# Kernel optimization log

Measured on AMD Instinct MI355X. Metric: run time of the kernel, lower is better.

The kernel has to match this reference:

```python
import jax, jax.numpy as jnp
import numpy as np

N = 50000      # nodes
E = 800000     # edges (before self loops)
D_IN = 128
D_H = 128
HEADS = 4
C = D_H // HEADS
D_OUT = 64
G = 50         # graphs in batch
EPS = 1e-5


def setup_inputs() -> dict:
    key = jax.random.key(0)
    ks = jax.random.split(key, 40)
    def rn(k, shape, scale=0.05):
        return jax.random.normal(k, shape, jnp.float32) * scale
    inp = {}
    inp['x'] = jax.random.normal(ks[0], (N, D_IN), jnp.float32)
    inp['edge_index'] = jax.random.randint(ks[1], (2, E), 0, N, dtype=jnp.int32)
    inp['batch'] = jnp.sort(jax.random.randint(ks[2], (N,), 0, G, dtype=jnp.int32))
    # GATConv 1 (in=D_IN, heads=4, out-per-head=C, concat)
    inp['gat1_W'] = rn(ks[3], (D_IN, D_H))
    inp['gat1_as'] = rn(ks[4], (HEADS, C))
    inp['gat1_ad'] = rn(ks[5], (HEADS, C))
    inp['gat1_b'] = rn(ks[6], (D_H,))
    # GATConv 2 (in=D_H)
    inp['gat2_W'] = rn(ks[7], (D_H, D_H))
    inp['gat2_as'] = rn(ks[8], (HEADS, C))
    inp['gat2_ad'] = rn(ks[9], (HEADS, C))
    inp['gat2_b'] = rn(ks[10], (D_H,))
    # SAGEConv 3/4/5: lin_l (aggregated neighbors, has bias), lin_r (root, no bias)
    for i, kk in zip((3, 4, 5), (11, 14, 17)):
        inp[f'sage{i}_Wl'] = rn(ks[kk], (D_H, D_H))
        inp[f'sage{i}_bl'] = rn(ks[kk + 1], (D_H,))
        inp[f'sage{i}_Wr'] = rn(ks[kk + 2], (D_H, D_H))
    # BatchNorms (training-mode batch statistics)
    for i in range(1, 6):
        inp[f'bn{i}_g'] = jnp.ones((D_H,), jnp.float32)
        inp[f'bn{i}_b'] = jnp.zeros((D_H,), jnp.float32)
    # residual projections + final fc
    inp['res1_W'] = rn(ks[20], (D_IN, D_H)); inp['res1_b'] = rn(ks[21], (D_H,))
    inp['res2_W'] = rn(ks[22], (D_H, D_H)); inp['res2_b'] = rn(ks[23], (D_H,))
    inp['fc_W'] = rn(ks[24], (D_H, D_OUT)); inp['fc_b'] = rn(ks[25], (D_OUT,))
    return inp


def _segsum(v, idx, n):
    return jax.ops.segment_sum(v, idx, num_segments=n)


def _gat(x, W, a_src, a_dst, b, src, dst):
    # PyG GATConv with self loops already appended to (src, dst).
    h = (x @ W).reshape(N, HEADS, C)
    es = jnp.einsum('nhc,hc->nh', h, a_src)           # [N,H]
    ed = jnp.einsum('nhc,hc->nh', h, a_dst)
    e = jax.nn.leaky_relu(es[src] + ed[dst], 0.2)     # [Etot,H]
    m = jax.ops.segment_max(e, dst, num_segments=N)
    m = jnp.where(jnp.isfinite(m), m, 0.0)
    w = jnp.exp(e - m[dst])
    z = _segsum(w, dst, N)
    alpha = w / jnp.maximum(z[dst], 1e-16)            # edge softmax over dst
    out = _segsum(h[src] * alpha[:, :, None], dst, N)  # [N,H,C]
    return out.reshape(N, D_H) + b


def _sage(x, Wl, bl, Wr, src, dst):
    # PyG SAGEConv(aggr='mean'): lin_l(mean_neighbors) + lin_r(x)
    deg = _segsum(jnp.ones((src.shape[0],), x.dtype), dst, N)
    mean = _segsum(x[src], dst, N) / jnp.maximum(deg, 1.0)[:, None]
    return mean @ Wl + bl + x @ Wr


def _bn(x, g, b):
    mu = x.mean(0)
    var = x.var(0)
    return g * (x - mu) * jax.lax.rsqrt(var + EPS) + b


def reference(x, edge_index, batch,
              gat1_W, gat1_as, gat1_ad, gat1_b,
              gat2_W, gat2_as, gat2_ad, gat2_b,
              sage3_Wl, sage3_bl, sage3_Wr,
              sage4_Wl, sage4_bl, sage4_Wr,
              sage5_Wl, sage5_bl, sage5_Wr,
              bn1_g, bn1_b, bn2_g, bn2_b, bn3_g, bn3_b, bn4_g, bn4_b, bn5_g, bn5_b,
              res1_W, res1_b, res2_W, res2_b, fc_W, fc_b):
    src, dst = edge_index[0], edge_index[1]
    loops = jnp.arange(N, dtype=edge_index.dtype)
    gsrc = jnp.concatenate([src, loops])   # GATConv adds self loops by default
    gdst = jnp.concatenate([dst, loops])
    lrelu = lambda v: jax.nn.leaky_relu(v, 0.2)

    res1 = x @ res1_W + res1_b
    h = _gat(x, gat1_W, gat1_as, gat1_ad, gat1_b, gsrc, gdst)
    h = lrelu(_bn(h, bn1_g, bn1_b) + res1)            # dropout = identity (eval)

    res2 = h @ res2_W + res2_b
    h = _gat(h, gat2_W, gat2_as, gat2_ad, gat2_b, gsrc, gdst)
    h = lrelu(_bn(h, bn2_g, bn2_b) + res2)

    h = lrelu(_bn(_sage(h, sage3_Wl, sage3_bl, sage3_Wr, src, dst), bn3_g, bn3_b))
    h = lrelu(_bn(_sage(h, sage4_Wl, sage4_bl, sage4_Wr, src, dst), bn4_g, bn4_b))
    h = lrelu(_bn(_sage(h, sage5_Wl, sage5_bl, sage5_Wr, src, dst), bn5_g, bn5_b))

    # global_mean_pool over graphs
    cnt = jax.ops.segment_sum(jnp.ones((N,), h.dtype), batch, num_segments=G)
    pooled = jax.ops.segment_sum(h, batch, num_segments=G) / jnp.maximum(cnt, 1.0)[:, None]
    return pooled @ fc_W + fc_b
```

## Files before the change

kernel.cpp:

```cpp
#include <hip/hip_runtime.h>
#include <math.h>
#include <stdint.h>

#define N_NODES 50000
#define N_EDGES 800000
#define D 128
#define GR 50
#define EPSV 1e-5f

typedef __attribute__((ext_vector_type(8))) short bf16x8;
typedef __attribute__((ext_vector_type(4))) float f32x4;

__device__ __forceinline__ float lrelu(float v){ return v > 0.f ? v : 0.2f*v; }

__device__ __forceinline__ unsigned int f2bf(float f){
  union { float f; uint32_t i; } v; v.f = f;
  uint32_t r = v.i + 0x7fffu + ((v.i >> 16) & 1u);
  return r >> 16;
}
__device__ __forceinline__ float2 bf2f2(uint32_t u){
  union { uint32_t i; float f; } a, b;
  a.i = u << 16;
  b.i = u & 0xffff0000u;
  return make_float2(a.f, b.f);
}

__global__ void k_countrank(const int* __restrict__ dst, int* __restrict__ deg,
                            int* __restrict__ rank){
  int e = blockIdx.x*256 + threadIdx.x;
  if (e < N_EDGES) rank[e] = atomicAdd(&deg[dst[e]], 1);
}
__global__ void k_scan1(const int* __restrict__ deg, int* __restrict__ bsum){
  __shared__ int s[256];
  int i = blockIdx.x*256 + threadIdx.x;
  int v = (i < N_NODES) ? deg[i] : 0;
  s[threadIdx.x] = v; __syncthreads();
  for (int off = 128; off > 0; off >>= 1){
    if (threadIdx.x < off) s[threadIdx.x] += s[threadIdx.x + off];
    __syncthreads();
  }
  if (threadIdx.x == 0) bsum[blockIdx.x] = s[0];
}
__global__ void k_scan2b(int* __restrict__ bsum, int nb, int* __restrict__ rowStart){
  __shared__ int s[256];
  int t = threadIdx.x;
  int v = (t < nb) ? bsum[t] : 0;
  s[t] = v; __syncthreads();
  for (int off = 1; off < 256; off <<= 1){
    int xv = (t >= off) ? s[t - off] : 0;
    __syncthreads();
    s[t] += xv;
    __syncthreads();
  }
  if (t < nb) bsum[t] = s[t] - v;
  if (t == 255) rowStart[N_NODES] = s[255];
}
__global__ void k_scan3(const int* __restrict__ deg, const int* __restrict__ bsum,
                        int* __restrict__ rowStart){
  __shared__ int s[256];
  int i = blockIdx.x*256 + threadIdx.x;
  int v = (i < N_NODES) ? deg[i] : 0;
  s[threadIdx.x] = v; __syncthreads();
  for (int off = 1; off < 256; off <<= 1){
    int xv = (threadIdx.x >= off) ? s[threadIdx.x - off] : 0;
    __syncthreads();
    s[threadIdx.x] += xv;
    __syncthreads();
  }
  if (i < N_NODES) rowStart[i] = bsum[blockIdx.x] + s[threadIdx.x] - v;
}
__global__ void k_scatter(const int* __restrict__ src, const int* __restrict__ dst,
                          const int* __restrict__ rank, const int* __restrict__ rowStart,
                          int* __restrict__ srcList){
  int e = blockIdx.x*256 + threadIdx.x;
  if (e < N_EDGES)
    srcList[rowStart[dst[e]] + rank[e]] = src[e];
}

__global__ void k_cast_x(const float* __restrict__ x, unsigned short* __restrict__ x16){
  int idx = blockIdx.x*256 + threadIdx.x;
  if (idx >= N_NODES*32) return;
  float4 v = *(const float4*)(x + (size_t)idx*4);
  uint2 pk;
  pk.x = f2bf(v.x) | (f2bf(v.y) << 16);
  pk.y = f2bf(v.z) | (f2bf(v.w) << 16);
  *(uint2*)(x16 + (size_t)idx*4) = pk;
}

struct WPack { const float* w[10]; };
__global__ void k_castw(WPack p, unsigned short* __restrict__ wt){
  int mat = blockIdx.x >> 6;
  int local = (blockIdx.x & 63)*256 + threadIdx.x;
  int c = local >> 7, k = local & 127;
  wt[(size_t)mat*16384 + c*128 + k] = (unsigned short)f2bf(p.w[mat][k*128 + c]);
}

__device__ __forceinline__ void stage_w(const unsigned short* __restrict__ wt,
                                        unsigned short* __restrict__ lds, int t){
  #pragma unroll
  for (int i = 0; i < 8; ++i){
    int ch = i*256 + t;
    int col = ch >> 4, kc = ch & 15;
    *(uint4*)(&lds[col*136 + kc*8]) = *(const uint4*)(wt + ((size_t)col << 7) + (kc << 3));
  }
}

__device__ __forceinline__ void load_a(const unsigned short* __restrict__ xrow,
                                       int quad, bf16x8 a[4]){
  #pragma unroll
  for (int ks = 0; ks < 4; ++ks)
    a[ks] = *(const bf16x8*)(xrow + ks*32 + quad*8);
}

__device__ __forceinline__ void mfma_regs(const bf16x8 a[4],
                                          const unsigned short* __restrict__ lds,
                                          int lane, f32x4 acc[8]){
  int quad = lane >> 4, m = lane & 15;
  #pragma unroll
  for (int ks = 0; ks < 4; ++ks){
    #pragma unroll
    for (int nt = 0; nt < 8; ++nt){
      bf16x8 b = *(const bf16x8*)(&lds[(nt*16 + m)*136 + ks*32 + quad*8]);
      acc[nt] = __builtin_amdgcn_mfma_f32_16x16x32_bf16(a[ks], b, acc[nt], 0, 0, 0);
    }
  }
}

__device__ __forceinline__ void epi_store16(f32x4 acc[8], const float* bias,
    unsigned short* __restrict__ ldsw, unsigned short* __restrict__ Y16,
    int rbase, int lane, int n){
  int quad = lane >> 4, m = lane & 15;
  #pragma unroll
  for (int nt = 0; nt < 8; ++nt){
    int col = nt*16 + m;
    float bv = bias ? bias[col] : 0.f;
    #pragma unroll
    for (int reg = 0; reg < 4; ++reg)
      ldsw[(quad*4 + reg)*132 + col] = (unsigned short)f2bf(acc[nt][reg] + bv);
  }
  int r = lane >> 2, seg = lane & 3;
  int grow = rbase + r;
  if (grow < n){
    unsigned short* gp = Y16 + (size_t)grow*128 + seg*32;
    #pragma unroll
    for (int j = 0; j < 4; ++j)
      *(uint4*)(gp + j*8) = *(const uint4*)(&ldsw[r*132 + seg*32 + j*8]);
  }
}

__global__ __launch_bounds__(256) void k_mgemm(const unsigned short* __restrict__ X16,
    const unsigned short* __restrict__ wt, const float* __restrict__ bias,
    unsigned short* __restrict__ Y16, int n){
  __shared__ __align__(16) unsigned short Wlds[128*136];
  int t = threadIdx.x, lane = t & 63, w = t >> 6;
  int quad = lane >> 4, m = lane & 15;
  int rbase = blockIdx.x*64 + w*16;
  int rowA = rbase + m; if (rowA >= n) rowA = n - 1;
  bf16x8 a[4];
  load_a(X16 + (size_t)rowA*128, quad, a);
  stage_w(wt, Wlds, t);
  f32x4 acc[8];
  #pragma unroll
  for (int nt = 0; nt < 8; ++nt){ acc[nt][0]=0.f; acc[nt][1]=0.f; acc[nt][2]=0.f; acc[nt][3]=0.f; }
  __syncthreads();
  mfma_regs(a, Wlds, lane, acc);
  __syncthreads();
  epi_store16(acc, bias, Wlds + w*2112, Y16, rbase, lane, n);
}

__global__ __launch_bounds__(256) void k_mgemm_gat(const unsigned short* __restrict__ X16,
    const unsigned short* __restrict__ wt, const float* __restrict__ as_,
    const float* __restrict__ ad_, unsigned short* __restrict__ H16,
    float* __restrict__ es, float* __restrict__ ed, int n){
  __shared__ __align__(16) unsigned short Wlds[128*136];
  int t = threadIdx.x, lane = t & 63, w = t >> 6;
  int quad = lane >> 4, m = lane & 15;
  int rbase = blockIdx.x*64 + w*16;
  int rowA = rbase + m; if (rowA >= n) rowA = n - 1;
  bf16x8 a[4];
  load_a(X16 + (size_t)rowA*128, quad, a);
  stage_w(wt, Wlds, t);
  f32x4 acc[8];
  #pragma unroll
  for (int nt = 0; nt < 8; ++nt){ acc[nt][0]=0.f; acc[nt][1]=0.f; acc[nt][2]=0.f; acc[nt][3]=0.f; }
  __syncthreads();
  mfma_regs(a, Wlds, lane, acc);

  float asv[8], adv[8];
  #pragma unroll
  for (int nt = 0; nt < 8; ++nt){ asv[nt] = as_[nt*16 + m]; adv[nt] = ad_[nt*16 + m]; }
  #pragma unroll
  for (int reg = 0; reg < 4; ++reg){
    int row = rbase + quad*4 + reg;
    float pe[4], pd[4];
    #pragma unroll
    for (int h = 0; h < 4; ++h){
      pe[h] = acc[2*h][reg]*asv[2*h] + acc[2*h+1][reg]*asv[2*h+1];
      pd[h] = acc[2*h][reg]*adv[2*h] + acc[2*h+1][reg]*adv[2*h+1];
    }
    #pragma unroll
    for (int h = 0; h < 4; ++h){
      pe[h] += __shfl_xor(pe[h], 1); pe[h] += __shfl_xor(pe[h], 2);
      pe[h] += __shfl_xor(pe[h], 4); pe[h] += __shfl_xor(pe[h], 8);
      pd[h] += __shfl_xor(pd[h], 1); pd[h] += __shfl_xor(pd[h], 2);
      pd[h] += __shfl_xor(pd[h], 4); pd[h] += __shfl_xor(pd[h], 8);
    }
    if (m == 0 && row < n){
      #pragma unroll
      for (int h = 0; h < 4; ++h){ es[row*4 + h] = pe[h]; ed[row*4 + h] = pd[h]; }
    }
  }
  __syncthreads();
  epi_store16(acc, nullptr, Wlds + w*2112, H16, rbase, lane, n);
}

__global__ __launch_bounds__(256) void k_mgemm2(const unsigned short* __restrict__ Xa,
    const unsigned short* __restrict__ wta, const unsigned short* __restrict__ Xb,
    const unsigned short* __restrict__ wtb, const float* __restrict__ bias,
    unsigned short* __restrict__ Y16, int n, float* __restrict__ bnpart){
  __shared__ __align__(16) unsigned short Wlds[128*136];
  __shared__ float wredS[4][128], wredQ[4][128];
  int t = threadIdx.x, lane = t & 63, w = t >> 6;
  int quad = lane >> 4, m = lane & 15;
  int rbase = blockIdx.x*64 + w*16;
  int rowA = rbase + m; if (rowA >= n) rowA = n - 1;
  bf16x8 aa[4], ab[4];
  load_a(Xa + (size_t)rowA*128, quad, aa);
  load_a(Xb + (size_t)rowA*128, quad, ab);
  stage_w(wta, Wlds, t);
  f32x4 acc[8];
  #pragma unroll
  for (int nt = 0; nt < 8; ++nt){ acc[nt][0]=0.f; acc[nt][1]=0.f; acc[nt][2]=0.f; acc[nt][3]=0.f; }
  __syncthreads();
  mfma_regs(aa, Wlds, lane, acc);
  __syncthreads();
  stage_w(wtb, Wlds, t);
  __syncthreads();
  mfma_regs(ab, Wlds, lane, acc);

  float colS[8], colQ[8];
  #pragma unroll
  for (int nt = 0; nt < 8; ++nt){
    float bv = bias[nt*16 + m];
    float s = 0.f, q = 0.f;
    #pragma unroll
    for (int reg = 0; reg < 4; ++reg){
      float o = acc[nt][reg] + bv;
      acc[nt][reg] = o;
      if (rbase + quad*4 + reg < n){ s += o; q += o*o; }
    }
    s += __shfl_xor(s, 16); s += __shfl_xor(s, 32);
    q += __shfl_xor(q, 16); q += __shfl_xor(q, 32);
    colS[nt] = s; colQ[nt] = q;
  }
  if (quad == 0){
    #pragma unroll
    for (int nt = 0; nt < 8; ++nt){
      wredS[w][nt*16 + m] = colS[nt];
      wredQ[w][nt*16 + m] = colQ[nt];
    }
  }
  __syncthreads();
  if (t < 128){
    float S = wredS[0][t] + wredS[1][t] + wredS[2][t] + wredS[3][t];
    float Q = wredQ[0][t] + wredQ[1][t] + wredQ[2][t] + wredQ[3][t];
    bnpart[(size_t)blockIdx.x*256 + t]       = S;
    bnpart[(size_t)blockIdx.x*256 + 128 + t] = Q;
  }
  epi_store16(acc, nullptr, Wlds + w*2112, Y16, rbase, lane, n);
}

__global__ void k_bnred(const float* __restrict__ part, int nblk,
                        float* __restrict__ sums){
  int g = blockIdx.x, t = threadIdx.x;
  int chunk = (nblk + 63) / 64;
  int b0 = g*chunk, b1 = min(nblk, b0 + chunk);
  float s = 0.f;
  for (int b = b0; b < b1; ++b) s += part[(size_t)b*256 + t];
  if (b0 < b1) atomicAdd(&sums[t], s);
}

__global__ __launch_bounds__(256) void k_gat(const uint4* __restrict__ h16,
    const float* __restrict__ es, const float* __restrict__ edv,
    const int* __restrict__ rowStart, const int* __restrict__ srcList,
    const float* __restrict__ bias, uint4* __restrict__ out16){
  int i = blockIdx.x*4 + (threadIdx.x >> 6);
  if (i >= N_NODES) return;
  int lane = threadIdx.x & 63;
  int sub = lane >> 4;
  int m   = lane & 15;
  int hd  = m >> 2;
  float edi = edv[i*4 + hd];
  float acc[8];
  #pragma unroll
  for (int j = 0; j < 8; ++j) acc[j] = 0.f;
  float z = 0.f;
  if (sub == 0){
    float ws = __expf(lrelu(es[i*4 + hd] + edi));
    uint4 u = h16[(size_t)i*16 + m];
    float2 v0=bf2f2(u.x), v1=bf2f2(u.y), v2=bf2f2(u.z), v3=bf2f2(u.w);
    acc[0]=v0.x*ws; acc[1]=v0.y*ws; acc[2]=v1.x*ws; acc[3]=v1.y*ws;
    acc[4]=v2.x*ws; acc[5]=v2.y*ws; acc[6]=v3.x*ws; acc[7]=v3.y*ws;
    z = ws;
  }
  int k0 = rowStart[i], ke = rowStart[i + 1];
  for (int k = k0; k < ke; k += 8){
    int e0 = k + sub, e1 = k + 4 + sub;
    int c0 = e0 < ke ? e0 : ke - 1;
    int c1 = e1 < ke ? e1 : ke - 1;
    int s0 = srcList[c0];
    int s1 = srcList[c1];
    uint4 u0 = h16[(size_t)s0*16 + m];
    uint4 u1 = h16[(size_t)s1*16 + m];
    float w0 = (e0 < ke) ? __expf(lrelu(es[s0*4 + hd] + edi)) : 0.f;
    float w1 = (e1 < ke) ? __expf(lrelu(es[s1*4 + hd] + edi)) : 0.f;
    z += w0 + w1;
    float2 a0=bf2f2(u0.x), a1=bf2f2(u0.y), a2=bf2f2(u0.z), a3=bf2f2(u0.w);
    float2 b0=bf2f2(u1.x), b1=bf2f2(u1.y), b2=bf2f2(u1.z), b3=bf2f2(u1.w);
    acc[0] += a0.x*w0 + b0.x*w1;  acc[1] += a0.y*w0 + b0.y*w1;
    acc[2] += a1.x*w0 + b1.x*w1;  acc[3] += a1.y*w0 + b1.y*w1;
    acc[4] += a2.x*w0 + b2.x*w1;  acc[5] += a2.y*w0 + b2.y*w1;
    acc[6] += a3.x*w0 + b3.x*w1;  acc[7] += a3.y*w0 + b3.y*w1;
  }
  #pragma unroll
  for (int j = 0; j < 8; ++j){
    acc[j] += __shfl_xor(acc[j], 16);
    acc[j] += __shfl_xor(acc[j], 32);
  }
  z += __shfl_xor(z, 16);
  z += __shfl_xor(z, 32);
  if (sub == 0){
    float inv = 1.f / z;
    float4 bv0 = *(const float4*)(bias + m*8);
    float4 bv1 = *(const float4*)(bias + m*8 + 4);
    uint4 pk;
    pk.x = f2bf(acc[0]*inv + bv0.x) | (f2bf(acc[1]*inv + bv0.y) << 16);
    pk.y = f2bf(acc[2]*inv + bv0.z) | (f2bf(acc[3]*inv + bv0.w) << 16);
    pk.z = f2bf(acc[4]*inv + bv1.x) | (f2bf(acc[5]*inv + bv1.y) << 16);
    pk.w = f2bf(acc[6]*inv + bv1.z) | (f2bf(acc[7]*inv + bv1.w) << 16);
    out16[(size_t)i*16 + m] = pk;
  }
}

__global__ __launch_bounds__(256) void k_sage_mean(const uint4* __restrict__ h16,
    const int* __restrict__ rowStart, const int* __restrict__ srcList,
    uint4* __restrict__ out16){
  int i = blockIdx.x*4 + (threadIdx.x >> 6);
  if (i >= N_NODES) return;
  int lane = threadIdx.x & 63;
  int sub = lane >> 4;
  int m   = lane & 15;
  float acc[8];
  #pragma unroll
  for (int j = 0; j < 8; ++j) acc[j] = 0.f;
  int k0 = rowStart[i], ke = rowStart[i + 1];
  for (int k = k0; k < ke; k += 8){
    int e0 = k + sub, e1 = k + 4 + sub;
    int c0 = e0 < ke ? e0 : ke - 1;
    int c1 = e1 < ke ? e1 : ke - 1;
    int s0 = srcList[c0];
    int s1 = srcList[c1];
    uint4 u0 = h16[(size_t)s0*16 + m];
    uint4 u1 = h16[(size_t)s1*16 + m];
    float w0 = (e0 < ke) ? 1.f : 0.f;
    float w1 = (e1 < ke) ? 1.f : 0.f;
    float2 a0=bf2f2(u0.x), a1=bf2f2(u0.y), a2=bf2f2(u0.z), a3=bf2f2(u0.w);
    float2 b0=bf2f2(u1.x), b1=bf2f2(u1.y), b2=bf2f2(u1.z), b3=bf2f2(u1.w);
    acc[0] += a0.x*w0 + b0.x*w1;  acc[1] += a0.y*w0 + b0.y*w1;
    acc[2] += a1.x*w0 + b1.x*w1;  acc[3] += a1.y*w0 + b1.y*w1;
    acc[4] += a2.x*w0 + b2.x*w1;  acc[5] += a2.y*w0 + b2.y*w1;
    acc[6] += a3.x*w0 + b3.x*w1;  acc[7] += a3.y*w0 + b3.y*w1;
  }
  #pragma unroll
  for (int j = 0; j < 8; ++j){
    acc[j] += __shfl_xor(acc[j], 16);
    acc[j] += __shfl_xor(acc[j], 32);
  }
  if (sub == 0){
    int dg = ke - k0;
    float inv = 1.f / (float)(dg > 0 ? dg : 1);
    uint4 pk;
    pk.x = f2bf(acc[0]*inv) | (f2bf(acc[1]*inv) << 16);
    pk.y = f2bf(acc[2]*inv) | (f2bf(acc[3]*inv) << 16);
    pk.z = f2bf(acc[4]*inv) | (f2bf(acc[5]*inv) << 16);
    pk.w = f2bf(acc[6]*inv) | (f2bf(acc[7]*inv) << 16);
    out16[(size_t)i*16 + m] = pk;
  }
}

__global__ __launch_bounds__(256) void k_bnstat(const unsigned int* __restrict__ x16,
                                                float* __restrict__ sums){
  int colu = threadIdx.x & 63;
  int ro   = threadIdx.x >> 6;
  float s0 = 0.f, s1 = 0.f, q0 = 0.f, q1 = 0.f;
  for (int r = blockIdx.x*4 + ro; r < N_NODES; r += gridDim.x*4){
    float2 v = bf2f2(x16[(size_t)r*64 + colu]);
    s0 += v.x; s1 += v.y; q0 += v.x*v.x; q1 += v.y*v.y;
  }
  __shared__ float rs0[256], rs1[256], rq0[256], rq1[256];
  int t = threadIdx.x;
  rs0[t] = s0; rs1[t] = s1; rq0[t] = q0; rq1[t] = q1;
  __syncthreads();
  if (t < 64){
    float S0 = rs0[t] + rs0[t+64] + rs0[t+128] + rs0[t+192];
    float S1 = rs1[t] + rs1[t+64] + rs1[t+128] + rs1[t+192];
    float Q0 = rq0[t] + rq0[t+64] + rq0[t+128] + rq0[t+192];
    float Q1 = rq1[t] + rq1[t+64] + rq1[t+128] + rq1[t+192];
    atomicAdd(&sums[2*t],       S0);
    atomicAdd(&sums[2*t + 1],   S1);
    atomicAdd(&sums[128 + 2*t],     Q0);
    atomicAdd(&sums[128 + 2*t + 1], Q1);
  }
}

__global__ void k_bnapply(const unsigned int* __restrict__ x16,
    const float* __restrict__ sums, const float* __restrict__ g,
    const float* __restrict__ b, const unsigned int* __restrict__ res16,
    unsigned int* __restrict__ y16){
  int f = blockIdx.x*256 + threadIdx.x;
  if (f >= N_NODES*32) return;
  int c = (f & 31) * 4;
  uint2 u = *(const uint2*)(x16 + (size_t)f*2);
  float2 vA = bf2f2(u.x), vB = bf2f2(u.y);
  float vv[4] = {vA.x, vA.y, vB.x, vB.y};
  float rr[4] = {0.f, 0.f, 0.f, 0.f};
  if (res16){
    uint2 ur = *(const uint2*)(res16 + (size_t)f*2);
    float2 rA = bf2f2(ur.x), rB = bf2f2(ur.y);
    rr[0]=rA.x; rr[1]=rA.y; rr[2]=rB.x; rr[3]=rB.y;
  }
  float o[4];
  const float invn = 1.f / (float)N_NODES;
  #pragma unroll
  for (int j = 0; j < 4; ++j){
    int cc = c + j;
    float mu  = sums[cc] * invn;
    float var = sums[128 + cc] * invn - mu*mu;
    float rs  = rsqrtf(var + EPSV);
    o[j] = lrelu((vv[j] - mu)*rs*g[cc] + b[cc] + rr[j]);
  }
  uint2 pk;
  pk.x = f2bf(o[0]) | (f2bf(o[1]) << 16);
  pk.y = f2bf(o[2]) | (f2bf(o[3]) << 16);
  *(uint2*)(y16 + (size_t)f*2) = pk;
}

__global__ __launch_bounds__(256) void k_pool(const unsigned int* __restrict__ h16,
    const int* __restrict__ batch, float* __restrict__ pooled,
    float* __restrict__ cnt){
  int colu = threadIdx.x & 63;
  int ro   = threadIdx.x >> 6;
  int base = blockIdx.x * 128;
  int g_cur = -1; float a0 = 0.f, a1 = 0.f, cacc = 0.f;
  for (int ii = 0; ii < 32; ++ii){
    int r = base + ro + ii*4;
    if (r >= N_NODES) break;
    int g = batch[r];
    if (g != g_cur){
      if (g_cur >= 0){
        atomicAdd(&pooled[g_cur*D + 2*colu],     a0);
        atomicAdd(&pooled[g_cur*D + 2*colu + 1], a1);
        if (colu == 0) atomicAdd(&cnt[g_cur], cacc);
      }
      a0 = 0.f; a1 = 0.f; cacc = 0.f; g_cur = g;
    }
    float2 v = bf2f2(h16[(size_t)r*64 + colu]);
    a0 += v.x; a1 += v.y; cacc += 1.f;
  }
  if (g_cur >= 0){
    atomicAdd(&pooled[g_cur*D + 2*colu],     a0);
    atomicAdd(&pooled[g_cur*D + 2*colu + 1], a1);
    if (colu == 0) atomicAdd(&cnt[g_cur], cacc);
  }
}

__global__ void k_fc(const float* __restrict__ pooled, const float* __restrict__ cnt,
    const float* __restrict__ W, const float* __restrict__ b, float* __restrict__ out){
  int idx = blockIdx.x*256 + threadIdx.x;
  if (idx >= GR*64) return;
  int g = idx >> 6, o = idx & 63;
  const float* p = pooled + g*D;
  float s = 0.f;
  for (int c2 = 0; c2 < D; ++c2) s += p[c2] * W[c2*64 + o];
  float inv = 1.f / fmaxf(cnt[g], 1.f);
  out[idx] = s*inv + b[o];
}

extern "C" void kernel_launch(void* const* d_in, const int* in_sizes, int n_in,
                              void* d_out, int out_size, void* d_ws, size_t ws_size,
                              hipStream_t stream){
  (void)in_sizes; (void)n_in; (void)out_size; (void)ws_size;
  const float* x       = (const float*)d_in[0];
  const int*   ei      = (const int*)  d_in[1];
  const int*   batch   = (const int*)  d_in[2];
  const float* gat1_W  = (const float*)d_in[3];
  const float* gat1_as = (const float*)d_in[4];
  const float* gat1_ad = (const float*)d_in[5];
  const float* gat1_b  = (const float*)d_in[6];
  const float* gat2_W  = (const float*)d_in[7];
  const float* gat2_as = (const float*)d_in[8];
  const float* gat2_ad = (const float*)d_in[9];
  const float* gat2_b  = (const float*)d_in[10];
  const float* s3_Wl   = (const float*)d_in[11];
  const float* s3_bl   = (const float*)d_in[12];
  const float* s3_Wr   = (const float*)d_in[13];
  const float* s4_Wl   = (const float*)d_in[14];
  const float* s4_bl   = (const float*)d_in[15];
  const float* s4_Wr   = (const float*)d_in[16];
  const float* s5_Wl   = (const float*)d_in[17];
  const float* s5_bl   = (const float*)d_in[18];
  const float* s5_Wr   = (const float*)d_in[19];
  const float* bn1_g = (const float*)d_in[20]; const float* bn1_b = (const float*)d_in[21];
  const float* bn2_g = (const float*)d_in[22]; const float* bn2_b = (const float*)d_in[23];
  const float* bn3_g = (const float*)d_in[24]; const float* bn3_b = (const float*)d_in[25];
  const float* bn4_g = (const float*)d_in[26]; const float* bn4_b = (const float*)d_in[27];
  const float* bn5_g = (const float*)d_in[28]; const float* bn5_b = (const float*)d_in[29];
  const float* res1_W = (const float*)d_in[30]; const float* res1_b = (const float*)d_in[31];
  const float* res2_W = (const float*)d_in[32]; const float* res2_b = (const float*)d_in[33];
  const float* fc_W   = (const float*)d_in[34]; const float* fc_b   = (const float*)d_in[35];
  float* out = (float*)d_out;

  char* ws = (char*)d_ws;
  size_t off = 0;
  auto alloc = [&](size_t bytes) -> void* {
    void* p = ws + off; off += (bytes + 255) & ~(size_t)255; return p;
  };
  const int mgrid = (N_NODES + 63) / 64;
  int*   rowStart = (int*)  alloc((N_NODES + 1) * 4);
  int*   deg      = (int*)  alloc((size_t)N_NODES * 4);
  int*   rank     = (int*)  alloc((size_t)N_EDGES * 4);
  int*   srcList  = (int*)  alloc((size_t)N_EDGES * 4);
  int*   bsum     = (int*)  alloc(256 * 4);
  float* bnsums   = (float*)alloc(5 * 256 * 4);
  float* pooled   = (float*)alloc(GR * D * 4);
  float* cnt      = (float*)alloc(64 * 4);
  float* es       = (float*)alloc((size_t)N_NODES * 4 * 4);
  float* edv      = (float*)alloc((size_t)N_NODES * 4 * 4);
  float* bnpart   = (float*)alloc((size_t)mgrid * 256 * 4);
  unsigned short* Wt16 = (unsigned short*)alloc(10 * 16384 * 2);
  unsigned short* HX   = (unsigned short*)alloc((size_t)N_NODES * D * 2);
  unsigned short* H16a = (unsigned short*)alloc((size_t)N_NODES * D * 2);
  unsigned short* HO   = (unsigned short*)alloc((size_t)N_NODES * D * 2);
  unsigned short* HR   = (unsigned short*)alloc((size_t)N_NODES * D * 2);

  const int* srcE = ei;
  const int* dstE = ei + N_EDGES;
  const int nb = (N_NODES + 255) / 256;
  const int egrid = (N_EDGES + 255) / 256;
  const int agrid = (N_NODES + 3) / 4;
  const int bgrid = (N_NODES*32 + 255) / 256;
  const int pgrid = (N_NODES + 127) / 128;

  hipMemsetAsync(deg, 0, (size_t)N_NODES*4, stream);
  hipMemsetAsync(bnsums, 0, (5*256 + GR*D + 64)*4, stream);
  k_countrank<<<egrid, 256, 0, stream>>>(dstE, deg, rank);
  k_scan1<<<nb, 256, 0, stream>>>(deg, bsum);
  k_scan2b<<<1, 256, 0, stream>>>(bsum, nb, rowStart);
  k_scan3<<<nb, 256, 0, stream>>>(deg, bsum, rowStart);
  k_scatter<<<egrid, 256, 0, stream>>>(srcE, dstE, rank, rowStart, srcList);

  WPack wp;
  wp.w[0]=res1_W; wp.w[1]=gat1_W; wp.w[2]=res2_W; wp.w[3]=gat2_W;
  wp.w[4]=s3_Wl;  wp.w[5]=s3_Wr;  wp.w[6]=s4_Wl;  wp.w[7]=s4_Wr;
  wp.w[8]=s5_Wl;  wp.w[9]=s5_Wr;
  k_castw<<<640, 256, 0, stream>>>(wp, Wt16);
  k_cast_x<<<bgrid, 256, 0, stream>>>(x, HX);

  k_mgemm<<<mgrid, 256, 0, stream>>>(HX, Wt16 + 0*16384, res1_b, HR, N_NODES);
  k_mgemm_gat<<<mgrid, 256, 0, stream>>>(HX, Wt16 + 1*16384, gat1_as, gat1_ad,
                                         H16a, es, edv, N_NODES);
  k_gat<<<agrid, 256, 0, stream>>>((const uint4*)H16a, es, edv, rowStart,
                                   srcList, gat1_b, (uint4*)HO);
  k_bnstat<<<256, 256, 0, stream>>>((const unsigned int*)HO, bnsums);
  k_bnapply<<<bgrid, 256, 0, stream>>>((const unsigned int*)HO, bnsums, bn1_g, bn1_b,
                                       (const unsigned int*)HR, (unsigned int*)H16a);

  k_mgemm<<<mgrid, 256, 0, stream>>>(H16a, Wt16 + 2*16384, res2_b, HR, N_NODES);
  k_mgemm_gat<<<mgrid, 256, 0, stream>>>(H16a, Wt16 + 3*16384, gat2_as, gat2_ad,
                                         HX, es, edv, N_NODES);
  k_gat<<<agrid, 256, 0, stream>>>((const uint4*)HX, es, edv, rowStart,
                                   srcList, gat2_b, (uint4*)HO);
  k_bnstat<<<256, 256, 0, stream>>>((const unsigned int*)HO, bnsums + 256);
  k_bnapply<<<bgrid, 256, 0, stream>>>((const unsigned int*)HO, bnsums + 256, bn2_g, bn2_b,
                                       (const unsigned int*)HR, (unsigned int*)H16a);

  k_sage_mean<<<agrid, 256, 0, stream>>>((const uint4*)H16a, rowStart, srcList,
                                         (uint4*)HX);
  k_mgemm2<<<mgrid, 256, 0, stream>>>(HX, Wt16 + 4*16384, H16a, Wt16 + 5*16384,
                                      s3_bl, HO, N_NODES, bnpart);
  k_bnred<<<64, 256, 0, stream>>>(bnpart, mgrid, bnsums + 512);
  k_bnapply<<<bgrid, 256, 0, stream>>>((const unsigned int*)HO, bnsums + 512, bn3_g, bn3_b,
                                       nullptr, (unsigned int*)H16a);

  k_sage_mean<<<agrid, 256, 0, stream>>>((const uint4*)H16a, rowStart, srcList,
                                         (uint4*)HX);
  k_mgemm2<<<mgrid, 256, 0, stream>>>(HX, Wt16 + 6*16384, H16a, Wt16 + 7*16384,
                                      s4_bl, HO, N_NODES, bnpart);
  k_bnred<<<64, 256, 0, stream>>>(bnpart, mgrid, bnsums + 768);
  k_bnapply<<<bgrid, 256, 0, stream>>>((const unsigned int*)HO, bnsums + 768, bn4_g, bn4_b,
                                       nullptr, (unsigned int*)H16a);

  k_sage_mean<<<agrid, 256, 0, stream>>>((const uint4*)H16a, rowStart, srcList,
                                         (uint4*)HX);
  k_mgemm2<<<mgrid, 256, 0, stream>>>(HX, Wt16 + 8*16384, H16a, Wt16 + 9*16384,
                                      s5_bl, HO, N_NODES, bnpart);
  k_bnred<<<64, 256, 0, stream>>>(bnpart, mgrid, bnsums + 1024);
  k_bnapply<<<bgrid, 256, 0, stream>>>((const unsigned int*)HO, bnsums + 1024, bn5_g, bn5_b,
                                       nullptr, (unsigned int*)H16a);

  k_pool<<<pgrid, 256, 0, stream>>>((const unsigned int*)H16a, batch, pooled, cnt);
  k_fc<<<(GR*64 + 255)/256, 256, 0, stream>>>(pooled, cnt, fc_W, fc_b, out);
}
```

Baseline: 628.4 us.

## Fuse residual and GAT GEMMs; fold BN statistics into persistent GAT aggregation

Merges the residual-projection GEMM and the GAT projection GEMM into one kernel, so the input tile is loaded once and the two weight matrices are staged into shared memory one after the other. The GAT aggregation kernel becomes a grid-stride persistent kernel with a fixed grid. It accumulates per-column sum and sum-of-squares of its outputs and writes per-block partials, which a small reduction kernel then combines. This drops the separate pass that reread the GAT output for BatchNorm statistics. The cost is higher register pressure in the dual GEMM, a larger partial buffer, and 32-bit index arithmetic in place of size_t.

```diff
diff --git a/kernel.cpp b/kernel.cpp
--- a/kernel.cpp
+++ b/kernel.cpp
@@ -7,6 +7,7 @@
 #define D 128
 #define GR 50
 #define EPSV 1e-5f
+#define GATGRID 2048
 
 typedef __attribute__((ext_vector_type(8))) short bf16x8;
 typedef __attribute__((ext_vector_type(4))) float f32x4;
@@ -148,9 +149,12 @@
   }
 }
 
-__global__ __launch_bounds__(256) void k_mgemm(const unsigned short* __restrict__ X16,
-    const unsigned short* __restrict__ wt, const float* __restrict__ bias,
-    unsigned short* __restrict__ Y16, int n){
+__global__ __launch_bounds__(256) void k_mgemm_dual(const unsigned short* __restrict__ X16,
+    const unsigned short* __restrict__ wtres, const unsigned short* __restrict__ wtgat,
+    const float* __restrict__ bres, const float* __restrict__ as_,
+    const float* __restrict__ ad_, unsigned short* __restrict__ R16,
+    unsigned short* __restrict__ H16, float* __restrict__ es, float* __restrict__ ed,
+    int n){
   __shared__ __align__(16) unsigned short Wlds[128*136];
   int t = threadIdx.x, lane = t & 63, w = t >> 6;
   int quad = lane >> 4, m = lane & 15;
@@ -158,33 +162,19 @@
   int rowA = rbase + m; if (rowA >= n) rowA = n - 1;
   bf16x8 a[4];
   load_a(X16 + (size_t)rowA*128, quad, a);
-  stage_w(wt, Wlds, t);
-  f32x4 acc[8];
-  #pragma unroll
-  for (int nt = 0; nt < 8; ++nt){ acc[nt][0]=0.f; acc[nt][1]=0.f; acc[nt][2]=0.f; acc[nt][3]=0.f; }
-  __syncthreads();
-  mfma_regs(a, Wlds, lane, acc);
-  __syncthreads();
-  epi_store16(acc, bias, Wlds + w*2112, Y16, rbase, lane, n);
-}
-
-__global__ __launch_bounds__(256) void k_mgemm_gat(const unsigned short* __restrict__ X16,
-    const unsigned short* __restrict__ wt, const float* __restrict__ as_,
-    const float* __restrict__ ad_, unsigned short* __restrict__ H16,
-    float* __restrict__ es, float* __restrict__ ed, int n){
-  __shared__ __align__(16) unsigned short Wlds[128*136];
-  int t = threadIdx.x, lane = t & 63, w = t >> 6;
-  int quad = lane >> 4, m = lane & 15;
-  int rbase = blockIdx.x*64 + w*16;
-  int rowA = rbase + m; if (rowA >= n) rowA = n - 1;
-  bf16x8 a[4];
-  load_a(X16 + (size_t)rowA*128, quad, a);
-  stage_w(wt, Wlds, t);
-  f32x4 acc[8];
-  #pragma unroll
-  for (int nt = 0; nt < 8; ++nt){ acc[nt][0]=0.f; acc[nt][1]=0.f; acc[nt][2]=0.f; acc[nt][3]=0.f; }
-  __syncthreads();
-  mfma_regs(a, Wlds, lane, acc);
+  stage_w(wtres, Wlds, t);
+  f32x4 accR[8], accG[8];
+  #pragma unroll
+  for (int nt = 0; nt < 8; ++nt){
+    accR[nt][0]=0.f; accR[nt][1]=0.f; accR[nt][2]=0.f; accR[nt][3]=0.f;
+    accG[nt][0]=0.f; accG[nt][1]=0.f; accG[nt][2]=0.f; accG[nt][3]=0.f;
+  }
+  __syncthreads();
+  mfma_regs(a, Wlds, lane, accR);
+  __syncthreads();
+  stage_w(wtgat, Wlds, t);
+  __syncthreads();
+  mfma_regs(a, Wlds, lane, accG);
 
   float asv[8], adv[8];
   #pragma unroll
@@ -195,8 +185,8 @@
     float pe[4], pd[4];
     #pragma unroll
     for (int h = 0; h < 4; ++h){
-      pe[h] = acc[2*h][reg]*asv[2*h] + acc[2*h+1][reg]*asv[2*h+1];
-      pd[h] = acc[2*h][reg]*adv[2*h] + acc[2*h+1][reg]*adv[2*h+1];
+      pe[h] = accG[2*h][reg]*asv[2*h] + accG[2*h+1][reg]*asv[2*h+1];
+      pd[h] = accG[2*h][reg]*adv[2*h] + accG[2*h+1][reg]*adv[2*h+1];
     }
     #pragma unroll
     for (int h = 0; h < 4; ++h){
@@ -211,7 +201,8 @@
     }
   }
   __syncthreads();
-  epi_store16(acc, nullptr, Wlds + w*2112, H16, rbase, lane, n);
+  epi_store16(accR, bres,    Wlds + w*2112, R16, rbase, lane, n);
+  epi_store16(accG, nullptr, Wlds + w*2112, H16, rbase, lane, n);
 }
 
 __global__ __launch_bounds__(256) void k_mgemm2(const unsigned short* __restrict__ Xa,
@@ -283,62 +274,88 @@
 __global__ __launch_bounds__(256) void k_gat(const uint4* __restrict__ h16,
     const float* __restrict__ es, const float* __restrict__ edv,
     const int* __restrict__ rowStart, const int* __restrict__ srcList,
-    const float* __restrict__ bias, uint4* __restrict__ out16){
-  int i = blockIdx.x*4 + (threadIdx.x >> 6);
-  if (i >= N_NODES) return;
-  int lane = threadIdx.x & 63;
+    const float* __restrict__ bias, uint4* __restrict__ out16,
+    float* __restrict__ bnpart){
+  __shared__ float wredS[4][128], wredQ[4][128];
+  int t = threadIdx.x;
+  int lane = t & 63, wv = t >> 6;
   int sub = lane >> 4;
   int m   = lane & 15;
   int hd  = m >> 2;
-  float edi = edv[i*4 + hd];
-  float acc[8];
-  #pragma unroll
-  for (int j = 0; j < 8; ++j) acc[j] = 0.f;
-  float z = 0.f;
+  float4 bv0 = *(const float4*)(bias + m*8);
+  float4 bv1 = *(const float4*)(bias + m*8 + 4);
+  float colS[8], colQ[8];
+  #pragma unroll
+  for (int j = 0; j < 8; ++j){ colS[j] = 0.f; colQ[j] = 0.f; }
+
+  for (int i = blockIdx.x*4 + wv; i < N_NODES; i += GATGRID*4){
+    float edi = edv[i*4 + hd];
+    float acc[8];
+    #pragma unroll
+    for (int j = 0; j < 8; ++j) acc[j] = 0.f;
+    float z = 0.f;
+    if (sub == 0){
+      float ws = __expf(lrelu(es[i*4 + hd] + edi));
+      uint4 u = h16[i*16 + m];
+      float2 v0=bf2f2(u.x), v1=bf2f2(u.y), v2=bf2f2(u.z), v3=bf2f2(u.w);
+      acc[0]=v0.x*ws; acc[1]=v0.y*ws; acc[2]=v1.x*ws; acc[3]=v1.y*ws;
+      acc[4]=v2.x*ws; acc[5]=v2.y*ws; acc[6]=v3.x*ws; acc[7]=v3.y*ws;
+      z = ws;
+    }
+    int k0 = rowStart[i], ke = rowStart[i + 1];
+    for (int k = k0; k < ke; k += 8){
+      int e0 = k + sub, e1 = k + 4 + sub;
+      int c0 = e0 < ke ? e0 : ke - 1;
+      int c1 = e1 < ke ? e1 : ke - 1;
+      int s0 = srcList[c0];
+      int s1 = srcList[c1];
+      uint4 u0 = h16[s0*16 + m];
+      uint4 u1 = h16[s1*16 + m];
+      float w0 = (e0 < ke) ? __expf(lrelu(es[s0*4 + hd] + edi)) : 0.f;
+      float w1 = (e1 < ke) ? __expf(lrelu(es[s1*4 + hd] + edi)) : 0.f;
+      z += w0 + w1;
+      float2 a0=bf2f2(u0.x), a1=bf2f2(u0.y), a2=bf2f2(u0.z), a3=bf2f2(u0.w);
+      float2 b0=bf2f2(u1.x), b1=bf2f2(u1.y), b2=bf2f2(u1.z), b3=bf2f2(u1.w);
+      acc[0] += a0.x*w0 + b0.x*w1;  acc[1] += a0.y*w0 + b0.y*w1;
+      acc[2] += a1.x*w0 + b1.x*w1;  acc[3] += a1.y*w0 + b1.y*w1;
+      acc[4] += a2.x*w0 + b2.x*w1;  acc[5] += a2.y*w0 + b2.y*w1;
+      acc[6] += a3.x*w0 + b3.x*w1;  acc[7] += a3.y*w0 + b3.y*w1;
+    }
+    #pragma unroll
+    for (int j = 0; j < 8; ++j){
+      acc[j] += __shfl_xor(acc[j], 16);
+      acc[j] += __shfl_xor(acc[j], 32);
+    }
+    z += __shfl_xor(z, 16);
+    z += __shfl_xor(z, 32);
+    if (sub == 0){
+      float inv = 1.f / z;
+      float o[8];
+      o[0]=acc[0]*inv+bv0.x; o[1]=acc[1]*inv+bv0.y; o[2]=acc[2]*inv+bv0.z; o[3]=acc[3]*inv+bv0.w;
+      o[4]=acc[4]*inv+bv1.x; o[5]=acc[5]*inv+bv1.y; o[6]=acc[6]*inv+bv1.z; o[7]=acc[7]*inv+bv1.w;
+      #pragma unroll
+      for (int j = 0; j < 8; ++j){ colS[j] += o[j]; colQ[j] += o[j]*o[j]; }
+      uint4 pk;
+      pk.x = f2bf(o[0]) | (f2bf(o[1]) << 16);
+      pk.y = f2bf(o[2]) | (f2bf(o[3]) << 16);
+      pk.z = f2bf(o[4]) | (f2bf(o[5]) << 16);
+      pk.w = f2bf(o[6]) | (f2bf(o[7]) << 16);
+      out16[i*16 + m] = pk;
+    }
+  }
   if (sub == 0){
-    float ws = __expf(lrelu(es[i*4 + hd] + edi));
-    uint4 u = h16[(size_t)i*16 + m];
-    float2 v0=bf2f2(u.x), v1=bf2f2(u.y), v2=bf2f2(u.z), v3=bf2f2(u.w);
-    acc[0]=v0.x*ws; acc[1]=v0.y*ws; acc[2]=v1.x*ws; acc[3]=v1.y*ws;
-    acc[4]=v2.x*ws; acc[5]=v2.y*ws; acc[6]=v3.x*ws; acc[7]=v3.y*ws;
-    z = ws;
-  }
-  int k0 = rowStart[i], ke = rowStart[i + 1];
-  for (int k = k0; k < ke; k += 8){
-    int e0 = k + sub, e1 = k + 4 + sub;
-    int c0 = e0 < ke ? e0 : ke - 1;
-    int c1 = e1 < ke ? e1 : ke - 1;
-    int s0 = srcList[c0];
-    int s1 = srcList[c1];
-    uint4 u0 = h16[(size_t)s0*16 + m];
-    uint4 u1 = h16[(size_t)s1*16 + m];
-    float w0 = (e0 < ke) ? __expf(lrelu(es[s0*4 + hd] + edi)) : 0.f;
-    float w1 = (e1 < ke) ? __expf(lrelu(es[s1*4 + hd] + edi)) : 0.f;
-    z += w0 + w1;
-    float2 a0=bf2f2(u0.x), a1=bf2f2(u0.y), a2=bf2f2(u0.z), a3=bf2f2(u0.w);
-    float2 b0=bf2f2(u1.x), b1=bf2f2(u1.y), b2=bf2f2(u1.z), b3=bf2f2(u1.w);
-    acc[0] += a0.x*w0 + b0.x*w1;  acc[1] += a0.y*w0 + b0.y*w1;
-    acc[2] += a1.x*w0 + b1.x*w1;  acc[3] += a1.y*w0 + b1.y*w1;
-    acc[4] += a2.x*w0 + b2.x*w1;  acc[5] += a2.y*w0 + b2.y*w1;
-    acc[6] += a3.x*w0 + b3.x*w1;  acc[7] += a3.y*w0 + b3.y*w1;
-  }
-  #pragma unroll
-  for (int j = 0; j < 8; ++j){
-    acc[j] += __shfl_xor(acc[j], 16);
-    acc[j] += __shfl_xor(acc[j], 32);
-  }
-  z += __shfl_xor(z, 16);
-  z += __shfl_xor(z, 32);
-  if (sub == 0){
-    float inv = 1.f / z;
-    float4 bv0 = *(const float4*)(bias + m*8);
-    float4 bv1 = *(const float4*)(bias + m*8 + 4);
-    uint4 pk;
-    pk.x = f2bf(acc[0]*inv + bv0.x) | (f2bf(acc[1]*inv + bv0.y) << 16);
-    pk.y = f2bf(acc[2]*inv + bv0.z) | (f2bf(acc[3]*inv + bv0.w) << 16);
-    pk.z = f2bf(acc[4]*inv + bv1.x) | (f2bf(acc[5]*inv + bv1.y) << 16);
-    pk.w = f2bf(acc[6]*inv + bv1.z) | (f2bf(acc[7]*inv + bv1.w) << 16);
-    out16[(size_t)i*16 + m] = pk;
+    #pragma unroll
+    for (int j = 0; j < 8; ++j){
+      wredS[wv][m*8 + j] = colS[j];
+      wredQ[wv][m*8 + j] = colQ[j];
+    }
+  }
+  __syncthreads();
+  if (t < 128){
+    float S = wredS[0][t] + wredS[1][t] + wredS[2][t] + wredS[3][t];
+    float Q = wredQ[0][t] + wredQ[1][t] + wredQ[2][t] + wredQ[3][t];
+    bnpart[(size_t)blockIdx.x*256 + t]       = S;
+    bnpart[(size_t)blockIdx.x*256 + 128 + t] = Q;
   }
 }
 
@@ -360,8 +377,8 @@
     int c1 = e1 < ke ? e1 : ke - 1;
     int s0 = srcList[c0];
     int s1 = srcList[c1];
-    uint4 u0 = h16[(size_t)s0*16 + m];
-    uint4 u1 = h16[(size_t)s1*16 + m];
+    uint4 u0 = h16[s0*16 + m];
+    uint4 u1 = h16[s1*16 + m];
     float w0 = (e0 < ke) ? 1.f : 0.f;
     float w1 = (e1 < ke) ? 1.f : 0.f;
     float2 a0=bf2f2(u0.x), a1=bf2f2(u0.y), a2=bf2f2(u0.z), a3=bf2f2(u0.w);
@@ -384,32 +401,7 @@
     pk.y = f2bf(acc[2]*inv) | (f2bf(acc[3]*inv) << 16);
     pk.z = f2bf(acc[4]*inv) | (f2bf(acc[5]*inv) << 16);
     pk.w = f2bf(acc[6]*inv) | (f2bf(acc[7]*inv) << 16);
-    out16[(size_t)i*16 + m] = pk;
-  }
-}
-
-__global__ __launch_bounds__(256) void k_bnstat(const unsigned int* __restrict__ x16,
-                                                float* __restrict__ sums){
-  int colu = threadIdx.x & 63;
-  int ro   = threadIdx.x >> 6;
-  float s0 = 0.f, s1 = 0.f, q0 = 0.f, q1 = 0.f;
-  for (int r = blockIdx.x*4 + ro; r < N_NODES; r += gridDim.x*4){
-    float2 v = bf2f2(x16[(size_t)r*64 + colu]);
-    s0 += v.x; s1 += v.y; q0 += v.x*v.x; q1 += v.y*v.y;
-  }
-  __shared__ float rs0[256], rs1[256], rq0[256], rq1[256];
-  int t = threadIdx.x;
-  rs0[t] = s0; rs1[t] = s1; rq0[t] = q0; rq1[t] = q1;
-  __syncthreads();
-  if (t < 64){
-    float S0 = rs0[t] + rs0[t+64] + rs0[t+128] + rs0[t+192];
-    float S1 = rs1[t] + rs1[t+64] + rs1[t+128] + rs1[t+192];
-    float Q0 = rq0[t] + rq0[t+64] + rq0[t+128] + rq0[t+192];
-    float Q1 = rq1[t] + rq1[t+64] + rq1[t+128] + rq1[t+192];
-    atomicAdd(&sums[2*t],       S0);
-    atomicAdd(&sums[2*t + 1],   S1);
-    atomicAdd(&sums[128 + 2*t],     Q0);
-    atomicAdd(&sums[128 + 2*t + 1], Q1);
+    out16[i*16 + m] = pk;
   }
 }
 
@@ -536,7 +528,7 @@
   float* cnt      = (float*)alloc(64 * 4);
   float* es       = (float*)alloc((size_t)N_NODES * 4 * 4);
   float* edv      = (float*)alloc((size_t)N_NODES * 4 * 4);
-  float* bnpart   = (float*)alloc((size_t)mgrid * 256 * 4);
+  float* bnpart   = (float*)alloc((size_t)GATGRID * 256 * 4);
   unsigned short* Wt16 = (unsigned short*)alloc(10 * 16384 * 2);
   unsigned short* HX   = (unsigned short*)alloc((size_t)N_NODES * D * 2);
   unsigned short* H16a = (unsigned short*)alloc((size_t)N_NODES * D * 2);
@@ -566,21 +558,21 @@
   k_castw<<<640, 256, 0, stream>>>(wp, Wt16);
   k_cast_x<<<bgrid, 256, 0, stream>>>(x, HX);
 
-  k_mgemm<<<mgrid, 256, 0, stream>>>(HX, Wt16 + 0*16384, res1_b, HR, N_NODES);
-  k_mgemm_gat<<<mgrid, 256, 0, stream>>>(HX, Wt16 + 1*16384, gat1_as, gat1_ad,
-                                         H16a, es, edv, N_NODES);
-  k_gat<<<agrid, 256, 0, stream>>>((const uint4*)H16a, es, edv, rowStart,
-                                   srcList, gat1_b, (uint4*)HO);
-  k_bnstat<<<256, 256, 0, stream>>>((const unsigned int*)HO, bnsums);
+  k_mgemm_dual<<<mgrid, 256, 0, stream>>>(HX, Wt16 + 0*16384, Wt16 + 1*16384,
+                                          res1_b, gat1_as, gat1_ad,
+                                          HR, H16a, es, edv, N_NODES);
+  k_gat<<<GATGRID, 256, 0, stream>>>((const uint4*)H16a, es, edv, rowStart,
+                                     srcList, gat1_b, (uint4*)HO, bnpart);
+  k_bnred<<<64, 256, 0, stream>>>(bnpart, GATGRID, bnsums);
   k_bnapply<<<bgrid, 256, 0, stream>>>((const unsigned int*)HO, bnsums, bn1_g, bn1_b,
                                        (const unsigned int*)HR, (unsigned int*)H16a);
 
-  k_mgemm<<<mgrid, 256, 0, stream>>>(H16a, Wt16 + 2*16384, res2_b, HR, N_NODES);
-  k_mgemm_gat<<<mgrid, 256, 0, stream>>>(H16a, Wt16 + 3*16384, gat2_as, gat2_ad,
-                                         HX, es, edv, N_NODES);
-  k_gat<<<agrid, 256, 0, stream>>>((const uint4*)HX, es, edv, rowStart,
-                                   srcList, gat2_b, (uint4*)HO);
-  k_bnstat<<<256, 256, 0, stream>>>((const unsigned int*)HO, bnsums + 256);
+  k_mgemm_dual<<<mgrid, 256, 0, stream>>>(H16a, Wt16 + 2*16384, Wt16 + 3*16384,
+                                          res2_b, gat2_as, gat2_ad,
+                                          HR, HX, es, edv, N_NODES);
+  k_gat<<<GATGRID, 256, 0, stream>>>((const uint4*)HX, es, edv, rowStart,
+                                     srcList, gat2_b, (uint4*)HO, bnpart);
+  k_bnred<<<64, 256, 0, stream>>>(bnpart, GATGRID, bnsums + 256);
   k_bnapply<<<bgrid, 256, 0, stream>>>((const unsigned int*)HO, bnsums + 256, bn2_g, bn2_b,
                                        (const unsigned int*)HR, (unsigned int*)H16a);
 
```

Result: faster. 611.2 us (-2.7%).
